# Performance work log

Measured on AMD Instinct MI355X. Metric: run time of the kernel, lower is better.

## Reference

```python
import jax, jax.numpy as jnp
import numpy as np

B, L, D, H, NB = 64, 30, 512, 8, 6
AS, MT = 18, 4096
T = 3 * L
HD = D // H
EPS = 1e-3  # keras LayerNormalization default epsilon
CONV_FEAT = 7 * 7 * 64  # 84 ->(8,s4) 20 ->(4,s2) 9 ->(3,s1) 7


def setup_inputs() -> dict:
    key = jax.random.key(0)
    ks = iter(jax.random.split(key, 64))
    r = lambda *s: jax.random.normal(next(ks), s, jnp.float32) * 0.02
    inp = {
        'rtgs': jax.random.normal(next(ks), (B, L, 1), jnp.float32),
        'states': jax.random.uniform(next(ks), (B, L, 84, 84, 4), jnp.float32) * 255.0,
        'actions': jax.random.randint(next(ks), (B, L, 1), 0, AS),
        'timesteps': jax.random.randint(next(ks), (B, 1, 1), 0, MT + 1),
        # rtg embedding
        'W_rtg': r(1, D), 'b_rtg': r(D),
        # state conv stem (HWIO)
        'conv1_w': r(8, 8, 4, 32), 'conv1_b': r(32),
        'conv2_w': r(4, 4, 32, 64), 'conv2_b': r(64),
        'conv3_w': r(3, 3, 64, 64), 'conv3_b': r(64),
        'dense_s_w': r(CONV_FEAT, D), 'dense_s_b': r(D),
        # action embedding table
        'emb_a': r(AS, D),
        # positional embeddings
        'abs_pos': r(1, MT + 1, D), 'rel_pos': r(1, T + 1, D),
        # decoder blocks (stacked over NB)
        'ln1_g': 1.0 + r(NB, D), 'ln1_b': r(NB, D),
        'Wk': r(NB, D, D), 'bk': r(NB, D),
        'Wq': r(NB, D, D), 'bq': r(NB, D),
        'Wv': r(NB, D, D), 'bv': r(NB, D),
        'ln2_g': 1.0 + r(NB, D), 'ln2_b': r(NB, D),
        'W1': r(NB, D, 4 * D), 'b1': r(NB, 4 * D),
        'W2': r(NB, 4 * D, D), 'b2': r(NB, D),
        # final norm + head (no bias)
        'lnf_g': 1.0 + r(D), 'lnf_b': r(D),
        'W_head': r(D, AS),
    }
    return inp


def _conv(x, w, b, stride):
    y = jax.lax.conv_general_dilated(x, w, (stride, stride), 'VALID',
                                     dimension_numbers=('NHWC', 'HWIO', 'NHWC'))
    return jax.nn.relu(y + b)


def _layernorm(x, g, b):
    m = x.mean(-1, keepdims=True)
    v = ((x - m) ** 2).mean(-1, keepdims=True)
    return (x - m) / jnp.sqrt(v + EPS) * g + b


def _attn(x, Wk, bk, Wq, bq, Wv, bv):
    Bx, Tx, C = x.shape
    split = lambda z: z.reshape(Bx, Tx, H, HD).transpose(0, 2, 1, 3)  # (B,H,T,hd)
    k, q, v = split(x @ Wk + bk), split(x @ Wq + bq), split(x @ Wv + bv)
    # NOTE: faithful to source: scores = K @ Q^T (not Q @ K^T)
    s = jnp.einsum('bhid,bhjd->bhij', k, q) / jnp.sqrt(jnp.float32(HD))
    mask = jnp.tril(jnp.ones((Tx, Tx), bool))
    s = jnp.where(mask, s, -jnp.inf)
    w = jax.nn.softmax(s, axis=-1)
    o = jnp.einsum('bhij,bhjd->bhid', w, v)
    return o.transpose(0, 2, 1, 3).reshape(Bx, Tx, C)


def reference(rtgs, states, actions, timesteps, W_rtg, b_rtg,
              conv1_w, conv1_b, conv2_w, conv2_b, conv3_w, conv3_b,
              dense_s_w, dense_s_b, emb_a, abs_pos, rel_pos,
              ln1_g, ln1_b, Wk, bk, Wq, bq, Wv, bv,
              ln2_g, ln2_b, W1, b1, W2, b2, lnf_g, lnf_b, W_head):
    # embeddings
    rtg_e = jnp.tanh(rtgs @ W_rtg + b_rtg)                       # (B,L,D)
    s = states.reshape(B * L, 84, 84, 4) / 255.0
    s = _conv(s, conv1_w, conv1_b, 4)
    s = _conv(s, conv2_w, conv2_b, 2)
    s = _conv(s, conv3_w, conv3_b, 1)
    st_e = jnp.tanh(s.reshape(B, L, -1) @ dense_s_w + dense_s_b)  # (B,L,D)
    a_e = jnp.tanh(emb_a[actions[..., 0]])                        # (B,L,D)
    # positional: abs gathered at start timestep + relative
    abs_e = abs_pos[0][timesteps[:, 0, 0]][:, None, :]            # (B,1,D)
    pos = rel_pos[:, :T, :] + abs_e                               # (B,3L,D)
    # interleave (rtg, state, action) per timestep
    tokens = jnp.stack([rtg_e, st_e, a_e], axis=2).reshape(B, T, D)
    x = tokens + pos
    for i in range(NB):
        h = _layernorm(x, ln1_g[i], ln1_b[i])
        x = x + _attn(h, Wk[i], bk[i], Wq[i], bq[i], Wv[i], bv[i])
        h = _layernorm(x, ln2_g[i], ln2_b[i])
        x = x + jax.nn.gelu(h @ W1[i] + b1[i], approximate=False) @ W2[i] + b2[i]
    x = _layernorm(x, lnf_g, lnf_b)
    logits = x @ W_head                                           # (B,3L,AS)
    return logits[:, 1::3, :]                                     # state positions -> (B,L,AS)
```

## Files before the change

### kernel.cpp

```cpp
#include <hip/hip_runtime.h>
#include <hip/hip_bf16.h>

typedef __attribute__((ext_vector_type(8))) __bf16 bf16x8;
typedef __attribute__((ext_vector_type(4))) float f32x4;

#define ACT_NONE 0
#define ACT_RELU 1
#define ACT_GELU 2
#define ACT_TANH 3
#define OUT_F32 0
#define OUT_BF16 1
#define OUT_ADD 2

__device__ __forceinline__ void gll16(const void* g, void* l) {
  __builtin_amdgcn_global_load_lds(
      reinterpret_cast<const __attribute__((address_space(1))) unsigned int*>(
          reinterpret_cast<unsigned long long>(g)),
      reinterpret_cast<__attribute__((address_space(3))) unsigned int*>(
          reinterpret_cast<unsigned long long>(l)),
      16, 0, 0);
}

__device__ __forceinline__ int xcd_swz(int bid, int n) {
  const int q = n >> 3, r = n & 7, x = bid & 7, o = bid >> 3;
  return (x < r ? x * (q + 1) : r * (q + 1) + (x - r) * q) + o;
}

template<int MODE, int K>
__device__ __forceinline__ size_t a_rowbase(int m) {
  if constexpr (MODE == 0) {
    return (size_t)m * K;
  } else if constexpr (MODE == 1) {
    int img = m / 400; int p = m - img * 400; int oy = p / 20; int ox = p - oy * 20;
    return (size_t)img * 28224 + oy * 1344 + ox * 16;
  } else if constexpr (MODE == 2) {
    int img = m / 81; int p = m - img * 81; int oy = p / 9; int ox = p - oy * 9;
    return (size_t)img * 12800 + oy * 1280 + ox * 64;
  } else {
    int img = m / 49; int p = m - img * 49; int oy = p / 7; int ox = p - oy * 7;
    return (size_t)img * 5184 + oy * 576 + ox * 64;
  }
}
template<int MODE>
__device__ __forceinline__ int f_koff(int kb) {
  if constexpr (MODE == 0) return kb;
  else if constexpr (MODE == 2) return (kb >> 7) * 640 + ((kb >> 5) & 3) * 32;
  else return kb + (kb / 192) * 384;
}

__device__ __forceinline__ bf16x8 ld8f(const float* f) {
  float4 a = *(const float4*)f;
  float4 b = *(const float4*)(f + 4);
  bf16x8 r;
  r[0] = (__bf16)a.x; r[1] = (__bf16)a.y; r[2] = (__bf16)a.z; r[3] = (__bf16)a.w;
  r[4] = (__bf16)b.x; r[5] = (__bf16)b.y; r[6] = (__bf16)b.z; r[7] = (__bf16)b.w;
  return r;
}

__device__ __forceinline__ float act_apply(float v, int ACT) {
  if (ACT == ACT_RELU) return fmaxf(v, 0.f);
  if (ACT == ACT_GELU) return 0.5f * v * (1.f + erff(v * 0.70710678118f));
  if (ACT == ACT_TANH) return tanhf(v);
  return v;
}

template<int MODE, int TM, int TN, int WM, int WN, int K, int ACT, int OUTM, int LDC, int NBLK, int SWZ>
__global__ __launch_bounds__(256) void gemm_k(const __bf16* __restrict__ A,
                                              const __bf16* __restrict__ BT,
                                              const float* __restrict__ bias,
                                              void* __restrict__ C) {
  constexpr int SM = TM / WM, SN = TN / WN;
  constexpr int AM = SM / 16, AN = SN / 16;
  constexpr int TA = TM / 64, TB = TN / 64;
  __shared__ __align__(16) __bf16 As[TM * 32];
  __shared__ __align__(16) __bf16 Bs[TN * 32];
  const int tid = threadIdx.x;
  const int wave = tid >> 6, lane = tid & 63;
  const int quad = lane >> 4, l16 = lane & 15;
  const int wr = wave % WM, wc = wave / WM;
  const int bid = SWZ ? xcd_swz(blockIdx.x, gridDim.x) : blockIdx.x;
  const int bn = bid % NBLK, bm = bid / NBLK;
  const int m0 = bm * TM, n0 = bn * TN;
  const int lrow = lane >> 2, lkc = lane & 3;

  const __bf16* ga[TA];
  const __bf16* gb[TB];
#pragma unroll
  for (int t = 0; t < TA; ++t)
    ga[t] = A + a_rowbase<MODE, K>(m0 + (wave + 4 * t) * 16 + lrow) + lkc * 8;
#pragma unroll
  for (int t = 0; t < TB; ++t)
    gb[t] = BT + (size_t)(n0 + (wave + 4 * t) * 16 + lrow) * K + lkc * 8;

  f32x4 acc[AM][AN] = {};
  for (int kt = 0; kt < K / 32; ++kt) {
    const int kb = kt * 32;
    const int fa = f_koff<MODE>(kb);
    __syncthreads();
#pragma unroll
    for (int t = 0; t < TA; ++t)
      gll16(ga[t] + fa, &As[(wave + 4 * t) * 16 * 32]);
#pragma unroll
    for (int t = 0; t < TB; ++t)
      gll16(gb[t] + kb, &Bs[(wave + 4 * t) * 16 * 32]);
    __syncthreads();
    bf16x8 af[AM], bf[AN];
#pragma unroll
    for (int mt = 0; mt < AM; ++mt)
      af[mt] = *(const bf16x8*)&As[(wr * SM + mt * 16 + l16) * 32 + quad * 8];
#pragma unroll
    for (int nt = 0; nt < AN; ++nt)
      bf[nt] = *(const bf16x8*)&Bs[(wc * SN + nt * 16 + l16) * 32 + quad * 8];
#pragma unroll
    for (int mt = 0; mt < AM; ++mt)
#pragma unroll
      for (int nt = 0; nt < AN; ++nt)
        acc[mt][nt] = __builtin_amdgcn_mfma_f32_16x16x32_bf16(af[mt], bf[nt], acc[mt][nt], 0, 0, 0);
  }

#pragma unroll
  for (int nt = 0; nt < AN; ++nt) {
    const int col = n0 + wc * SN + nt * 16 + l16;
    const float bvl = bias[col];
#pragma unroll
    for (int mt = 0; mt < AM; ++mt) {
#pragma unroll
      for (int r = 0; r < 4; ++r) {
        const int row = m0 + wr * SM + mt * 16 + quad * 4 + r;
        float v = act_apply(acc[mt][nt][r] + bvl, ACT);
        const size_t off = (size_t)row * LDC + col;
        if constexpr (OUTM == OUT_F32) ((float*)C)[off] = v;
        else if constexpr (OUTM == OUT_BF16) ((__bf16*)C)[off] = (__bf16)v;
        else ((float*)C)[off] += v;
      }
    }
  }
}

__global__ __launch_bounds__(256) void conv1_k(const float* __restrict__ A,
                                               const __bf16* __restrict__ BT,
                                               const float* __restrict__ bias,
                                               __bf16* __restrict__ C) {
  __shared__ __align__(16) __bf16 As[128 * 32];
  __shared__ __align__(16) __bf16 Bs[32 * 32];
  const int tid = threadIdx.x;
  const int wave = tid >> 6, lane = tid & 63;
  const int quad = lane >> 4, l16 = lane & 15;
  const int m0 = xcd_swz(blockIdx.x, gridDim.x) * 128;
  const int lrow = lane >> 2, lkc = lane & 3;
  const int r0 = tid >> 2, k0o = (tid & 3) * 8;
  const int r1 = r0 + 64;
  const size_t ar0 = a_rowbase<1, 256>(m0 + r0);
  const size_t ar1 = a_rowbase<1, 256>(m0 + r1);
  const __bf16* gB = BT + (size_t)(wave * 16 + lrow) * 256 + lkc * 8;

  f32x4 acc[2][2] = {};
  bf16x8 a0 = ld8f(A + ar0 + k0o);
  bf16x8 a1 = ld8f(A + ar1 + k0o);
  for (int kt = 0; kt < 8; ++kt) {
    const int kb = kt * 32;
    __syncthreads();
    if (wave < 2) gll16(gB + kb, &Bs[wave * 16 * 32]);
    *(bf16x8*)&As[r0 * 32 + k0o] = a0;
    *(bf16x8*)&As[r1 * 32 + k0o] = a1;
    __syncthreads();
    if (kt < 7) {
      const int fa = (kt + 1) * 336;
      a0 = ld8f(A + ar0 + fa + k0o);
      a1 = ld8f(A + ar1 + fa + k0o);
    }
    bf16x8 af[2], bf[2];
#pragma unroll
    for (int mt = 0; mt < 2; ++mt)
      af[mt] = *(const bf16x8*)&As[(wave * 32 + mt * 16 + l16) * 32 + quad * 8];
#pragma unroll
    for (int nt = 0; nt < 2; ++nt)
      bf[nt] = *(const bf16x8*)&Bs[(nt * 16 + l16) * 32 + quad * 8];
#pragma unroll
    for (int mt = 0; mt < 2; ++mt)
#pragma unroll
      for (int nt = 0; nt < 2; ++nt)
        acc[mt][nt] = __builtin_amdgcn_mfma_f32_16x16x32_bf16(af[mt], bf[nt], acc[mt][nt], 0, 0, 0);
  }
#pragma unroll
  for (int nt = 0; nt < 2; ++nt) {
    const int col = nt * 16 + l16;
    const float bvl = bias[col];
#pragma unroll
    for (int mt = 0; mt < 2; ++mt) {
#pragma unroll
      for (int r = 0; r < 4; ++r) {
        const int row = m0 + wave * 32 + mt * 16 + quad * 4 + r;
        C[(size_t)row * 32 + col] = (__bf16)fmaxf(acc[mt][nt][r] + bvl, 0.f);
      }
    }
  }
}

template<typename TO>
__global__ void transpose_pad(const float* __restrict__ src, TO* __restrict__ dst,
                              int R, int C, int Cpad, long long sz, long long dz, float scale) {
  src += blockIdx.z * sz; dst += blockIdx.z * dz;
  __shared__ float t[32][33];
  const int tx = threadIdx.x, ty = threadIdx.y;
  const int r0 = blockIdx.x * 32, c0 = blockIdx.y * 32;
  for (int i = ty; i < 32; i += 8) {
    int r = r0 + i, c = c0 + tx;
    t[i][tx] = (r < R && c < C) ? src[(size_t)r * C + c] : 0.f;
  }
  __syncthreads();
  for (int i = ty; i < 32; i += 8) {
    int c = c0 + i, r = r0 + tx;
    if (c < Cpad && r < R)
      dst[(size_t)c * R + r] = (c < C) ? (TO)(t[tx][i] * scale) : (TO)0.f;
  }
}

__global__ void transpose_qkv(const float* __restrict__ Wk_, const float* __restrict__ Wq_,
                              const float* __restrict__ Wv_, __bf16* __restrict__ dst) {
  const int z = blockIdx.z, which = z / 6, i = z - which * 6;
  const float* src = (which == 0 ? Wk_ : which == 1 ? Wq_ : Wv_) + (size_t)i * 512 * 512;
  __bf16* d = dst + (size_t)i * 1536 * 512 + (size_t)which * 512 * 512;
  __shared__ float t[32][33];
  const int tx = threadIdx.x, ty = threadIdx.y;
  const int r0 = blockIdx.x * 32, c0 = blockIdx.y * 32;
  for (int j = ty; j < 32; j += 8)
    t[j][tx] = src[(size_t)(r0 + j) * 512 + c0 + tx];
  __syncthreads();
  for (int j = ty; j < 32; j += 8)
    d[(size_t)(c0 + j) * 512 + r0 + tx] = (__bf16)t[tx][j];
}

__global__ void biascat_k(const float* bk, const float* bq, const float* bv, float* dst) {
  const int i = blockIdx.x;
  for (int d = threadIdx.x; d < 512; d += 256) {
    dst[i * 1536 + d] = bk[i * 512 + d];
    dst[i * 1536 + 512 + d] = bq[i * 512 + d];
    dst[i * 1536 + 1024 + d] = bv[i * 512 + d];
  }
}

__global__ void embed_k(const float* __restrict__ rtgs, const int* __restrict__ actions,
                        const int* __restrict__ timesteps, const float* __restrict__ W_rtg,
                        const float* __restrict__ b_rtg, const float* __restrict__ emb_a,
                        const float* __restrict__ abs_pos, const float* __restrict__ rel_pos,
                        const float* __restrict__ ste, float* __restrict__ x) {
  const int idx = blockIdx.x * 256 + threadIdx.x;
  const int d = idx & 511; const int rb = idx >> 9;
  const int b = rb / 90, t = rb - b * 90;
  const int l = t / 3, r = t - l * 3;
  const float pos = rel_pos[t * 512 + d] + abs_pos[(size_t)timesteps[b] * 512 + d];
  float tok;
  if (r == 0) tok = tanhf(rtgs[b * 30 + l] * W_rtg[d] + b_rtg[d]);
  else if (r == 1) tok = ste[(size_t)(b * 30 + l) * 512 + d];
  else tok = tanhf(emb_a[actions[b * 30 + l] * 512 + d]);
  x[idx] = tok + pos;
}

__global__ __launch_bounds__(256) void ln_k(const float* __restrict__ x, const float* __restrict__ g,
                                            const float* __restrict__ bb, __bf16* __restrict__ h) {
  const int row = blockIdx.x * 4 + (threadIdx.x >> 6);
  const int lane = threadIdx.x & 63;
  const float* xr = x + (size_t)row * 512;
  float4 a = *(const float4*)&xr[lane * 8];
  float4 c = *(const float4*)&xr[lane * 8 + 4];
  float vv[8] = {a.x, a.y, a.z, a.w, c.x, c.y, c.z, c.w};
  float s = 0.f, q = 0.f;
#pragma unroll
  for (int j = 0; j < 8; ++j) { s += vv[j]; q += vv[j] * vv[j]; }
  for (int o = 32; o; o >>= 1) { s += __shfl_xor(s, o); q += __shfl_xor(q, o); }
  const float mean = s * (1.f / 512.f);
  const float var = q * (1.f / 512.f) - mean * mean;
  const float rstd = rsqrtf(var + 1e-3f);
  float4 g1 = *(const float4*)&g[lane * 8];
  float4 g2 = *(const float4*)&g[lane * 8 + 4];
  float4 b1 = *(const float4*)&bb[lane * 8];
  float4 b2 = *(const float4*)&bb[lane * 8 + 4];
  float gg[8] = {g1.x, g1.y, g1.z, g1.w, g2.x, g2.y, g2.z, g2.w};
  float bbv[8] = {b1.x, b1.y, b1.z, b1.w, b2.x, b2.y, b2.z, b2.w};
  bf16x8 ov;
#pragma unroll
  for (int j = 0; j < 8; ++j)
    ov[j] = (__bf16)((vv[j] - mean) * rstd * gg[j] + bbv[j]);
  *(bf16x8*)&h[(size_t)row * 512 + lane * 8] = ov;
}

__global__ __launch_bounds__(256) void attn_k(const __bf16* __restrict__ qkv, float* __restrict__ x) {
  __shared__ __align__(16) char smem[64512];
  __bf16* kS = (__bf16*)smem;
  __bf16* qS = (__bf16*)(smem + 13824);
  __bf16* wS = (__bf16*)smem;
  float* sS = (float*)(smem + 27648);
  __bf16* vT = (__bf16*)(smem + 27648);

  const int tid = threadIdx.x;
  const int b = blockIdx.x >> 3, h = blockIdx.x & 7;
  const int wave = tid >> 6, lane = tid & 63, quad = lane >> 4, l16 = lane & 15;
  const size_t rowbase = (size_t)b * 90 * 1536 + h * 64;

  bf16x8 vreg[3];
#pragma unroll
  for (int it = 0; it < 3; ++it) {
    const int c = tid + it * 256, t = c >> 3, d8 = (c & 7) * 8;
#pragma unroll
    for (int j = 0; j < 8; ++j) vreg[it][j] = (__bf16)0.f;
    if (t < 90) vreg[it] = *(const bf16x8*)(qkv + rowbase + (size_t)t * 1536 + 1024 + d8);
  }

  for (int c = tid; c < 768; c += 256) {
    const int t = c >> 3, d8 = (c & 7) * 8;
    bf16x8 kv, qv;
#pragma unroll
    for (int j = 0; j < 8; ++j) { kv[j] = (__bf16)0.f; qv[j] = (__bf16)0.f; }
    if (t < 90) {
      const __bf16* src = qkv + rowbase + (size_t)t * 1536 + d8;
      kv = *(const bf16x8*)src;
      qv = *(const bf16x8*)(src + 512);
    }
    *(bf16x8*)&kS[t * 72 + d8] = kv;
    *(bf16x8*)&qS[t * 72 + d8] = qv;
  }
  __syncthreads();

  for (int tt = wave; tt < 36; tt += 4) {
    const int it = tt / 6, jt = tt - it * 6;
    f32x4 acc = {0.f, 0.f, 0.f, 0.f};
#pragma unroll
    for (int ks = 0; ks < 2; ++ks) {
      bf16x8 af = *(const bf16x8*)&kS[(it * 16 + l16) * 72 + ks * 32 + quad * 8];
      bf16x8 bq = *(const bf16x8*)&qS[(jt * 16 + l16) * 72 + ks * 32 + quad * 8];
      acc = __builtin_amdgcn_mfma_f32_16x16x32_bf16(af, bq, acc, 0, 0, 0);
    }
    const int col = jt * 16 + l16;
#pragma unroll
    for (int r = 0; r < 4; ++r) {
      const int row = it * 16 + quad * 4 + r;
      sS[row * 96 + col] = (col <= row && col < 90) ? acc[r] * 0.125f : -1e30f;
    }
  }
  __syncthreads();

  for (int row = wave; row < 96; row += 4) {
    const float e0 = sS[row * 96 + lane];
    const float e1 = (lane < 32) ? sS[row * 96 + 64 + lane] : -1e30f;
    float m = fmaxf(e0, e1);
    for (int o = 32; o; o >>= 1) m = fmaxf(m, __shfl_xor(m, o));
    const float p0 = __expf(e0 - m);
    const float p1 = (lane < 32) ? __expf(e1 - m) : 0.f;
    float s = p0 + p1;
    for (int o = 32; o; o >>= 1) s += __shfl_xor(s, o);
    const float inv = 1.f / s;
    wS[row * 104 + lane] = (__bf16)(p0 * inv);
    if (lane < 32) wS[row * 104 + 64 + lane] = (__bf16)(p1 * inv);
  }
  __syncthreads();

#pragma unroll
  for (int it = 0; it < 3; ++it) {
    const int c = tid + it * 256, t = c >> 3, d8 = (c & 7) * 8;
#pragma unroll
    for (int j = 0; j < 8; ++j) vT[(d8 + j) * 104 + t] = vreg[it][j];
  }
  __syncthreads();

  for (int tt = wave; tt < 24; tt += 4) {
    const int it = tt >> 2, dt = tt & 3;
    f32x4 acc = {0.f, 0.f, 0.f, 0.f};
#pragma unroll
    for (int ks = 0; ks < 3; ++ks) {
      bf16x8 aw = *(const bf16x8*)&wS[(it * 16 + l16) * 104 + ks * 32 + quad * 8];
      bf16x8 bv = *(const bf16x8*)&vT[(dt * 16 + l16) * 104 + ks * 32 + quad * 8];
      acc = __builtin_amdgcn_mfma_f32_16x16x32_bf16(aw, bv, acc, 0, 0, 0);
    }
    const int d = dt * 16 + l16;
#pragma unroll
    for (int r = 0; r < 4; ++r) {
      const int i = it * 16 + quad * 4 + r;
      if (i < 90) {
        float* p = x + (size_t)(b * 90 + i) * 512 + h * 64 + d;
        *p += acc[r];
      }
    }
  }
}

__global__ __launch_bounds__(64) void head_k(const float* __restrict__ x, const float* __restrict__ g,
                                             const float* __restrict__ bb, const float* __restrict__ whT,
                                             float* __restrict__ out) {
  const int m = blockIdx.x;
  const int b = m / 30, l = m - b * 30;
  const float* xr = x + (size_t)(b * 90 + 3 * l + 1) * 512;
  const int lane = threadIdx.x;
  float4 a = *(const float4*)&xr[lane * 8];
  float4 c = *(const float4*)&xr[lane * 8 + 4];
  float vv[8] = {a.x, a.y, a.z, a.w, c.x, c.y, c.z, c.w};
  float s = 0.f, q = 0.f;
#pragma unroll
  for (int j = 0; j < 8; ++j) { s += vv[j]; q += vv[j] * vv[j]; }
  for (int o = 32; o; o >>= 1) { s += __shfl_xor(s, o); q += __shfl_xor(q, o); }
  const float mean = s * (1.f / 512.f);
  const float var = q * (1.f / 512.f) - mean * mean;
  const float rstd = rsqrtf(var + 1e-3f);
  float4 g1 = *(const float4*)&g[lane * 8];
  float4 g2 = *(const float4*)&g[lane * 8 + 4];
  float4 b1 = *(const float4*)&bb[lane * 8];
  float4 b2 = *(const float4*)&bb[lane * 8 + 4];
  float gg[8] = {g1.x, g1.y, g1.z, g1.w, g2.x, g2.y, g2.z, g2.w};
  float bbv[8] = {b1.x, b1.y, b1.z, b1.w, b2.x, b2.y, b2.z, b2.w};
#pragma unroll
  for (int j = 0; j < 8; ++j)
    vv[j] = (vv[j] - mean) * rstd * gg[j] + bbv[j];
  for (int aa = 0; aa < 18; ++aa) {
    float4 w1v = *(const float4*)&whT[aa * 512 + lane * 8];
    float4 w2v = *(const float4*)&whT[aa * 512 + lane * 8 + 4];
    float ww[8] = {w1v.x, w1v.y, w1v.z, w1v.w, w2v.x, w2v.y, w2v.z, w2v.w};
    float d = 0.f;
#pragma unroll
    for (int j = 0; j < 8; ++j) d += vv[j] * ww[j];
    for (int o = 32; o; o >>= 1) d += __shfl_xor(d, o);
    if (lane == 0) out[m * 18 + aa] = d;
  }
}

extern "C" void kernel_launch(void* const* d_in, const int* in_sizes, int n_in,
                              void* d_out, int out_size, void* d_ws, size_t ws_size,
                              hipStream_t stream) {
  const float* rtgs = (const float*)d_in[0];
  const float* states = (const float*)d_in[1];
  const int* actions = (const int*)d_in[2];
  const int* timesteps = (const int*)d_in[3];
  const float* W_rtg = (const float*)d_in[4];
  const float* b_rtg = (const float*)d_in[5];
  const float* conv1_w = (const float*)d_in[6];
  const float* conv1_b = (const float*)d_in[7];
  const float* conv2_w = (const float*)d_in[8];
  const float* conv2_b = (const float*)d_in[9];
  const float* conv3_w = (const float*)d_in[10];
  const float* conv3_b = (const float*)d_in[11];
  const float* dense_s_w = (const float*)d_in[12];
  const float* dense_s_b = (const float*)d_in[13];
  const float* emb_a = (const float*)d_in[14];
  const float* abs_pos = (const float*)d_in[15];
  const float* rel_pos = (const float*)d_in[16];
  const float* ln1_g = (const float*)d_in[17];
  const float* ln1_b = (const float*)d_in[18];
  const float* Wk = (const float*)d_in[19];
  const float* bk = (const float*)d_in[20];
  const float* Wq = (const float*)d_in[21];
  const float* bq = (const float*)d_in[22];
  const float* Wv = (const float*)d_in[23];
  const float* bv = (const float*)d_in[24];
  const float* ln2_g = (const float*)d_in[25];
  const float* ln2_b = (const float*)d_in[26];
  const float* W1 = (const float*)d_in[27];
  const float* b1 = (const float*)d_in[28];
  const float* W2 = (const float*)d_in[29];
  const float* b2 = (const float*)d_in[30];
  const float* lnf_g = (const float*)d_in[31];
  const float* lnf_b = (const float*)d_in[32];
  const float* W_head = (const float*)d_in[33];
  float* out = (float*)d_out;

  char* W = (char*)d_ws;
  float* x = (float*)(W + 0);
  __bf16* h = (__bf16*)(W + 11796480);
  __bf16* qkvT = (__bf16*)(W + 17694720);
  __bf16* w1T = (__bf16*)(W + 27131904);
  __bf16* w2T = (__bf16*)(W + 39714816);
  __bf16* dswT = (__bf16*)(W + 52297728);
  __bf16* c1wT = (__bf16*)(W + 55508992);
  __bf16* c2wT = (__bf16*)(W + 55574528);
  __bf16* c3wT = (__bf16*)(W + 55705600);
  float* whT = (float*)(W + 55853056);
  float* bqkv = (float*)(W + 55889920);
  __bf16* c1out = (__bf16*)(W + 55926784);
  __bf16* c2out = (__bf16*)(W + 105078784);
  __bf16* c3out = (__bf16*)(W + 55926784);
  float* ste = (float*)(W + 67969024);
  __bf16* qkvb = (__bf16*)(W + 55926784);
  __bf16* mlph = (__bf16*)(W + 73621504);

  const dim3 tb(32, 8);
  transpose_pad<__bf16><<<dim3(8, 4, 1), tb, 0, stream>>>(conv1_w, c1wT, 256, 32, 128, 0, 0, 1.f / 255.f);
  transpose_pad<__bf16><<<dim3(16, 4, 1), tb, 0, stream>>>(conv2_w, c2wT, 512, 64, 128, 0, 0, 1.f);
  transpose_pad<__bf16><<<dim3(18, 4, 1), tb, 0, stream>>>(conv3_w, c3wT, 576, 64, 128, 0, 0, 1.f);
  transpose_pad<__bf16><<<dim3(98, 16, 1), tb, 0, stream>>>(dense_s_w, dswT, 3136, 512, 512, 0, 0, 1.f);
  transpose_qkv<<<dim3(16, 16, 18), tb, 0, stream>>>(Wk, Wq, Wv, qkvT);
  transpose_pad<__bf16><<<dim3(16, 64, 6), tb, 0, stream>>>(W1, w1T, 512, 2048, 2048, 512 * 2048, 2048 * 512, 1.f);
  transpose_pad<__bf16><<<dim3(64, 16, 6), tb, 0, stream>>>(W2, w2T, 2048, 512, 512, 2048 * 512, 512 * 2048, 1.f);
  transpose_pad<float><<<dim3(16, 1, 1), tb, 0, stream>>>(W_head, whT, 512, 18, 18, 0, 0, 1.f);
  biascat_k<<<6, 256, 0, stream>>>(bk, bq, bv, bqkv);

  conv1_k<<<6000, 256, 0, stream>>>(states, c1wT, conv1_b, c1out);
  gemm_k<2, 128, 64, 2, 2, 512, ACT_RELU, OUT_BF16, 64, 1, 1><<<1215, 256, 0, stream>>>(c1out, c2wT, conv2_b, c2out);
  gemm_k<3, 128, 64, 2, 2, 576, ACT_RELU, OUT_BF16, 64, 1, 1><<<735, 256, 0, stream>>>(c2out, c3wT, conv3_b, c3out);
  gemm_k<0, 64, 64, 2, 2, 3136, ACT_TANH, OUT_F32, 512, 8, 1><<<240, 256, 0, stream>>>(c3out, dswT, dense_s_b, (void*)ste);

  embed_k<<<11520, 256, 0, stream>>>(rtgs, actions, timesteps, W_rtg, b_rtg, emb_a, abs_pos, rel_pos, ste, x);

  for (int i = 0; i < 6; ++i) {
    ln_k<<<1440, 256, 0, stream>>>(x, ln1_g + i * 512, ln1_b + i * 512, h);
    gemm_k<0, 128, 128, 2, 2, 512, ACT_NONE, OUT_BF16, 1536, 12, 1><<<540, 256, 0, stream>>>(
        h, qkvT + (size_t)i * 1536 * 512, bqkv + i * 1536, qkvb);
    attn_k<<<512, 256, 0, stream>>>(qkvb, x);
    ln_k<<<1440, 256, 0, stream>>>(x, ln2_g + i * 512, ln2_b + i * 512, h);
    gemm_k<0, 128, 128, 2, 2, 512, ACT_GELU, OUT_BF16, 2048, 16, 1><<<720, 256, 0, stream>>>(
        h, w1T + (size_t)i * 2048 * 512, b1 + i * 2048, mlph);
    gemm_k<0, 64, 64, 2, 2, 2048, ACT_NONE, OUT_ADD, 512, 8, 1><<<720, 256, 0, stream>>>(
        mlph, w2T + (size_t)i * 2048 * 512, b2 + i * 512, x);
  }

  head_k<<<1920, 64, 0, stream>>>(x, lnf_g, lnf_b, whT, out);
}
```

Measured before the change: 1.305 ms.

## Fuse QKV projection into attention kernel with per-head weight layout

Removes the standalone QKV GEMM and the qkv buffer round-trip. Each attention block (one per batch and head) now computes its own 96x192 K/Q/V slice from the layernormed activations, then writes K and Q into shared memory and transposes V. QKV weights and biases are re-laid out per head (K, Q, V interleaved in 192-column groups), and the token dimension is padded from 90 to 96 so each batch covers whole 16-row tiles. The tradeoff is that each block streams the full 512-deep reduction itself, which gives less weight reuse across batches than the large tiled GEMM. The padding also adds about 7% more rows to every other kernel.

```diff
diff --git a/kernel.cpp b/kernel.cpp
--- a/kernel.cpp
+++ b/kernel.cpp
@@ -220,23 +220,27 @@
                               const float* __restrict__ Wv_, __bf16* __restrict__ dst) {
   const int z = blockIdx.z, which = z / 6, i = z - which * 6;
   const float* src = (which == 0 ? Wk_ : which == 1 ? Wq_ : Wv_) + (size_t)i * 512 * 512;
-  __bf16* d = dst + (size_t)i * 1536 * 512 + (size_t)which * 512 * 512;
+  __bf16* d = dst + (size_t)i * 1536 * 512;
   __shared__ float t[32][33];
   const int tx = threadIdx.x, ty = threadIdx.y;
   const int r0 = blockIdx.x * 32, c0 = blockIdx.y * 32;
   for (int j = ty; j < 32; j += 8)
     t[j][tx] = src[(size_t)(r0 + j) * 512 + c0 + tx];
   __syncthreads();
-  for (int j = ty; j < 32; j += 8)
-    d[(size_t)(c0 + j) * 512 + r0 + tx] = (__bf16)t[tx][j];
+  for (int j = ty; j < 32; j += 8) {
+    const int c = c0 + j;
+    const int row = ((c >> 6) * 192) + which * 64 + (c & 63);
+    d[(size_t)row * 512 + r0 + tx] = (__bf16)t[tx][j];
+  }
 }
 
 __global__ void biascat_k(const float* bk, const float* bq, const float* bv, float* dst) {
   const int i = blockIdx.x;
   for (int d = threadIdx.x; d < 512; d += 256) {
-    dst[i * 1536 + d] = bk[i * 512 + d];
-    dst[i * 1536 + 512 + d] = bq[i * 512 + d];
-    dst[i * 1536 + 1024 + d] = bv[i * 512 + d];
+    const int g = (d >> 6) * 192 + (d & 63);
+    dst[i * 1536 + g] = bk[i * 512 + d];
+    dst[i * 1536 + g + 64] = bq[i * 512 + d];
+    dst[i * 1536 + g + 128] = bv[i * 512 + d];
   }
 }
 
@@ -247,7 +251,8 @@
                         const float* __restrict__ ste, float* __restrict__ x) {
   const int idx = blockIdx.x * 256 + threadIdx.x;
   const int d = idx & 511; const int rb = idx >> 9;
-  const int b = rb / 90, t = rb - b * 90;
+  const int b = rb / 96, t = rb - b * 96;
+  if (t >= 90) { x[idx] = 0.f; return; }
   const int l = t / 3, r = t - l * 3;
   const float pos = rel_pos[t * 512 + d] + abs_pos[(size_t)timesteps[b] * 512 + d];
   float tok;
@@ -285,57 +290,89 @@
   *(bf16x8*)&h[(size_t)row * 512 + lane * 8] = ov;
 }
 
-__global__ __launch_bounds__(256) void attn_k(const __bf16* __restrict__ qkv, float* __restrict__ x) {
+__global__ __launch_bounds__(256) void qkvattn_k(const __bf16* __restrict__ A,
+                                                 const __bf16* __restrict__ BTh,
+                                                 const float* __restrict__ bias,
+                                                 float* __restrict__ x) {
   __shared__ __align__(16) char smem[64512];
   __bf16* kS = (__bf16*)smem;
   __bf16* qS = (__bf16*)(smem + 13824);
   __bf16* wS = (__bf16*)smem;
   float* sS = (float*)(smem + 27648);
   __bf16* vT = (__bf16*)(smem + 27648);
+  __bf16* As = (__bf16*)(smem + 27648);
+  __bf16* Bs = (__bf16*)(smem + 27648 + 6144);
 
   const int tid = threadIdx.x;
   const int b = blockIdx.x >> 3, h = blockIdx.x & 7;
   const int wave = tid >> 6, lane = tid & 63, quad = lane >> 4, l16 = lane & 15;
-  const size_t rowbase = (size_t)b * 90 * 1536 + h * 64;
-
-  bf16x8 vreg[3];
-#pragma unroll
-  for (int it = 0; it < 3; ++it) {
-    const int c = tid + it * 256, t = c >> 3, d8 = (c & 7) * 8;
-#pragma unroll
-    for (int j = 0; j < 8; ++j) vreg[it][j] = (__bf16)0.f;
-    if (t < 90) vreg[it] = *(const bf16x8*)(qkv + rowbase + (size_t)t * 1536 + 1024 + d8);
-  }
-
-  for (int c = tid; c < 768; c += 256) {
-    const int t = c >> 3, d8 = (c & 7) * 8;
-    bf16x8 kv, qv;
-#pragma unroll
-    for (int j = 0; j < 8; ++j) { kv[j] = (__bf16)0.f; qv[j] = (__bf16)0.f; }
-    if (t < 90) {
-      const __bf16* src = qkv + rowbase + (size_t)t * 1536 + d8;
-      kv = *(const bf16x8*)src;
-      qv = *(const bf16x8*)(src + 512);
-    }
-    *(bf16x8*)&kS[t * 72 + d8] = kv;
-    *(bf16x8*)&qS[t * 72 + d8] = qv;
+  const int wr = wave & 1, wc = wave >> 1;
+  const int lrow = lane >> 2, lkc = lane & 3;
+
+  const __bf16* ga0 = A + (size_t)(b * 96 + wave * 16 + lrow) * 512 + lkc * 8;
+  const __bf16* ga1 = A + (size_t)(b * 96 + ((wave & 1) + 4) * 16 + lrow) * 512 + lkc * 8;
+  const __bf16* gbp[3];
+#pragma unroll
+  for (int t = 0; t < 3; ++t)
+    gbp[t] = BTh + (size_t)(h * 192 + (wave + 4 * t) * 16 + lrow) * 512 + lkc * 8;
+
+  f32x4 acc[3][6] = {};
+  for (int kt = 0; kt < 16; ++kt) {
+    const int kb = kt * 32;
+    __syncthreads();
+    gll16(ga0 + kb, &As[wave * 16 * 32]);
+    if (wave < 2) gll16(ga1 + kb, &As[(wave + 4) * 16 * 32]);
+#pragma unroll
+    for (int t = 0; t < 3; ++t)
+      gll16(gbp[t] + kb, &Bs[(wave + 4 * t) * 16 * 32]);
+    __syncthreads();
+    bf16x8 af[3], bq[6];
+#pragma unroll
+    for (int mt = 0; mt < 3; ++mt)
+      af[mt] = *(const bf16x8*)&As[(wr * 48 + mt * 16 + l16) * 32 + quad * 8];
+#pragma unroll
+    for (int nt = 0; nt < 6; ++nt)
+      bq[nt] = *(const bf16x8*)&Bs[(wc * 96 + nt * 16 + l16) * 32 + quad * 8];
+#pragma unroll
+    for (int mt = 0; mt < 3; ++mt)
+#pragma unroll
+      for (int nt = 0; nt < 6; ++nt)
+        acc[mt][nt] = __builtin_amdgcn_mfma_f32_16x16x32_bf16(af[mt], bq[nt], acc[mt][nt], 0, 0, 0);
+  }
+
+#pragma unroll
+  for (int nt = 0; nt < 6; ++nt) {
+    const int col = wc * 96 + nt * 16 + l16;
+    if (col < 128) {
+      const float bvl = bias[h * 192 + col];
+#pragma unroll
+      for (int mt = 0; mt < 3; ++mt) {
+#pragma unroll
+        for (int r = 0; r < 4; ++r) {
+          const int row = wr * 48 + mt * 16 + quad * 4 + r;
+          const float v = acc[mt][nt][r] + bvl;
+          if (col < 64) kS[row * 72 + col] = (__bf16)v;
+          else qS[row * 72 + (col - 64)] = (__bf16)v;
+        }
+      }
+    }
   }
   __syncthreads();
 
   for (int tt = wave; tt < 36; tt += 4) {
     const int it = tt / 6, jt = tt - it * 6;
-    f32x4 acc = {0.f, 0.f, 0.f, 0.f};
+    f32x4 sacc = {0.f, 0.f, 0.f, 0.f};
 #pragma unroll
     for (int ks = 0; ks < 2; ++ks) {
       bf16x8 af = *(const bf16x8*)&kS[(it * 16 + l16) * 72 + ks * 32 + quad * 8];
       bf16x8 bq = *(const bf16x8*)&qS[(jt * 16 + l16) * 72 + ks * 32 + quad * 8];
-      acc = __builtin_amdgcn_mfma_f32_16x16x32_bf16(af, bq, acc, 0, 0, 0);
+      sacc = __builtin_amdgcn_mfma_f32_16x16x32_bf16(af, bq, sacc, 0, 0, 0);
     }
     const int col = jt * 16 + l16;
 #pragma unroll
     for (int r = 0; r < 4; ++r) {
       const int row = it * 16 + quad * 4 + r;
-      sS[row * 96 + col] = (col <= row && col < 90) ? acc[r] * 0.125f : -1e30f;
+      sS[row * 96 + col] = (col <= row && col < 90) ? sacc[r] * 0.125f : -1e30f;
     }
   }
   __syncthreads();
@@ -355,30 +392,39 @@
   }
   __syncthreads();
 
-#pragma unroll
-  for (int it = 0; it < 3; ++it) {
-    const int c = tid + it * 256, t = c >> 3, d8 = (c & 7) * 8;
-#pragma unroll
-    for (int j = 0; j < 8; ++j) vT[(d8 + j) * 104 + t] = vreg[it][j];
+  if (wc == 1) {
+#pragma unroll
+    for (int nt = 2; nt < 6; ++nt) {
+      const int vd = nt * 16 + l16 - 32;
+      const float bvl = bias[h * 192 + 128 + vd];
+#pragma unroll
+      for (int mt = 0; mt < 3; ++mt) {
+#pragma unroll
+        for (int r = 0; r < 4; ++r) {
+          const int row = wr * 48 + mt * 16 + quad * 4 + r;
+          vT[vd * 104 + row] = (__bf16)(acc[mt][nt][r] + bvl);
+        }
+      }
+    }
   }
   __syncthreads();
 
   for (int tt = wave; tt < 24; tt += 4) {
     const int it = tt >> 2, dt = tt & 3;
-    f32x4 acc = {0.f, 0.f, 0.f, 0.f};
+    f32x4 pacc = {0.f, 0.f, 0.f, 0.f};
 #pragma unroll
     for (int ks = 0; ks < 3; ++ks) {
       bf16x8 aw = *(const bf16x8*)&wS[(it * 16 + l16) * 104 + ks * 32 + quad * 8];
       bf16x8 bv = *(const bf16x8*)&vT[(dt * 16 + l16) * 104 + ks * 32 + quad * 8];
-      acc = __builtin_amdgcn_mfma_f32_16x16x32_bf16(aw, bv, acc, 0, 0, 0);
+      pacc = __builtin_amdgcn_mfma_f32_16x16x32_bf16(aw, bv, pacc, 0, 0, 0);
     }
     const int d = dt * 16 + l16;
 #pragma unroll
     for (int r = 0; r < 4; ++r) {
       const int i = it * 16 + quad * 4 + r;
       if (i < 90) {
-        float* p = x + (size_t)(b * 90 + i) * 512 + h * 64 + d;
-        *p += acc[r];
+        float* p = x + (size_t)(b * 96 + i) * 512 + h * 64 + d;
+        *p += pacc[r];
       }
     }
   }
@@ -389,7 +435,7 @@
                                              float* __restrict__ out) {
   const int m = blockIdx.x;
   const int b = m / 30, l = m - b * 30;
-  const float* xr = x + (size_t)(b * 90 + 3 * l + 1) * 512;
+  const float* xr = x + (size_t)(b * 96 + 3 * l + 1) * 512;
   const int lane = threadIdx.x;
   float4 a = *(const float4*)&xr[lane * 8];
   float4 c = *(const float4*)&xr[lane * 8 + 4];
@@ -463,22 +509,21 @@
 
   char* W = (char*)d_ws;
   float* x = (float*)(W + 0);
-  __bf16* h = (__bf16*)(W + 11796480);
-  __bf16* qkvT = (__bf16*)(W + 17694720);
-  __bf16* w1T = (__bf16*)(W + 27131904);
-  __bf16* w2T = (__bf16*)(W + 39714816);
-  __bf16* dswT = (__bf16*)(W + 52297728);
-  __bf16* c1wT = (__bf16*)(W + 55508992);
-  __bf16* c2wT = (__bf16*)(W + 55574528);
-  __bf16* c3wT = (__bf16*)(W + 55705600);
-  float* whT = (float*)(W + 55853056);
-  float* bqkv = (float*)(W + 55889920);
-  __bf16* c1out = (__bf16*)(W + 55926784);
-  __bf16* c2out = (__bf16*)(W + 105078784);
-  __bf16* c3out = (__bf16*)(W + 55926784);
-  float* ste = (float*)(W + 67969024);
-  __bf16* qkvb = (__bf16*)(W + 55926784);
-  __bf16* mlph = (__bf16*)(W + 73621504);
+  __bf16* h = (__bf16*)(W + 12582912);
+  __bf16* qkvT = (__bf16*)(W + 18874368);
+  __bf16* w1T = (__bf16*)(W + 28311552);
+  __bf16* w2T = (__bf16*)(W + 40894464);
+  __bf16* dswT = (__bf16*)(W + 53477376);
+  __bf16* c1wT = (__bf16*)(W + 56688640);
+  __bf16* c2wT = (__bf16*)(W + 56754176);
+  __bf16* c3wT = (__bf16*)(W + 56885248);
+  float* whT = (float*)(W + 57032704);
+  float* bqkv = (float*)(W + 57069568);
+  __bf16* c1out = (__bf16*)(W + 57106432);
+  __bf16* c2out = (__bf16*)(W + 106258432);
+  __bf16* c3out = (__bf16*)(W + 57106432);
+  float* ste = (float*)(W + 69148672);
+  __bf16* mlph = (__bf16*)(W + 57106432);
 
   const dim3 tb(32, 8);
   transpose_pad<__bf16><<<dim3(8, 4, 1), tb, 0, stream>>>(conv1_w, c1wT, 256, 32, 128, 0, 0, 1.f / 255.f);
@@ -496,17 +541,15 @@
   gemm_k<3, 128, 64, 2, 2, 576, ACT_RELU, OUT_BF16, 64, 1, 1><<<735, 256, 0, stream>>>(c2out, c3wT, conv3_b, c3out);
   gemm_k<0, 64, 64, 2, 2, 3136, ACT_TANH, OUT_F32, 512, 8, 1><<<240, 256, 0, stream>>>(c3out, dswT, dense_s_b, (void*)ste);
 
-  embed_k<<<11520, 256, 0, stream>>>(rtgs, actions, timesteps, W_rtg, b_rtg, emb_a, abs_pos, rel_pos, ste, x);
+  embed_k<<<12288, 256, 0, stream>>>(rtgs, actions, timesteps, W_rtg, b_rtg, emb_a, abs_pos, rel_pos, ste, x);
 
   for (int i = 0; i < 6; ++i) {
-    ln_k<<<1440, 256, 0, stream>>>(x, ln1_g + i * 512, ln1_b + i * 512, h);
-    gemm_k<0, 128, 128, 2, 2, 512, ACT_NONE, OUT_BF16, 1536, 12, 1><<<540, 256, 0, stream>>>(
-        h, qkvT + (size_t)i * 1536 * 512, bqkv + i * 1536, qkvb);
-    attn_k<<<512, 256, 0, stream>>>(qkvb, x);
-    ln_k<<<1440, 256, 0, stream>>>(x, ln2_g + i * 512, ln2_b + i * 512, h);
-    gemm_k<0, 128, 128, 2, 2, 512, ACT_GELU, OUT_BF16, 2048, 16, 1><<<720, 256, 0, stream>>>(
+    ln_k<<<1536, 256, 0, stream>>>(x, ln1_g + i * 512, ln1_b + i * 512, h);
+    qkvattn_k<<<512, 256, 0, stream>>>(h, qkvT + (size_t)i * 1536 * 512, bqkv + i * 1536, x);
+    ln_k<<<1536, 256, 0, stream>>>(x, ln2_g + i * 512, ln2_b + i * 512, h);
+    gemm_k<0, 128, 128, 2, 2, 512, ACT_GELU, OUT_BF16, 2048, 16, 1><<<768, 256, 0, stream>>>(
         h, w1T + (size_t)i * 2048 * 512, b1 + i * 2048, mlph);
-    gemm_k<0, 64, 64, 2, 2, 2048, ACT_NONE, OUT_ADD, 512, 8, 1><<<720, 256, 0, stream>>>(
+    gemm_k<0, 64, 64, 2, 2, 2048, ACT_NONE, OUT_ADD, 512, 8, 1><<<768, 256, 0, stream>>>(
         mlph, w2T + (size_t)i * 2048 * 512, b2 + i * 512, x);
   }
 
```

Result: no change. 1.294 ms (-0.8%).
